# Optimization experiments

Hardware: AMD Instinct MI355X
Metric: run time of the kernel (lower is better)

The kernel has to match this reference:

```python
import jax, jax.numpy as jnp
import numpy as np

N, DIM = 32768, 2048
SPARSITY = 0.05
K = max(1, int(N * SPARSITY))  # 1638


def setup_inputs() -> dict:
    key = jax.random.key(0)
    ks = jax.random.split(key, 6)
    s = 1.0 / np.sqrt(DIM)
    return {
        "x": jax.random.normal(ks[0], (N, DIM), dtype=jnp.float32),
        "W1": jax.random.uniform(ks[1], (DIM, DIM), jnp.float32, -s, s),
        "b1": jax.random.uniform(ks[2], (DIM,), jnp.float32, -s, s),
        "W2": jax.random.uniform(ks[3], (DIM, DIM), jnp.float32, -s, s),
        "b2": jax.random.uniform(ks[4], (DIM,), jnp.float32, -s, s),
        "Wg": jax.random.uniform(ks[5], (DIM,), jnp.float32, -s, s),
        "bg": jnp.zeros((), jnp.float32),
    }


def reference(x, W1, b1, W2, b2, Wg, bg):
    # gate scores per row: [N]
    gate_scores = x @ Wg + bg
    # select top-k rows (k is static)
    _, top_idx = jax.lax.top_k(gate_scores, K)
    # gather active rows and run the 2-layer MLP only on them
    active_x = x[top_idx]                                   # [K, DIM]
    h = jax.nn.relu(active_x @ W1 + b1)
    active_out = h @ W2 + b2                                # [K, DIM]
    # scatter results back into a zero output; row order is irrelevant
    output = jnp.zeros_like(x).at[top_idx].set(active_out)
    mask = jnp.zeros((x.shape[0],), x.dtype).at[top_idx].set(1.0)
    return output, mask
```

## Files before the change

### kernel.cpp

```cpp
#include <hip/hip_runtime.h>

#define N_ROWS 32768
#define DIM    2048
#define KSEL   1638
#define MPAD   1664
#define GTILE  416

typedef __attribute__((ext_vector_type(4))) float          f32x4;
typedef __attribute__((ext_vector_type(4))) unsigned short us4;
typedef __attribute__((ext_vector_type(8))) unsigned short us8;
typedef __bf16 bf16x8 __attribute__((ext_vector_type(8)));

__device__ __forceinline__ unsigned short f2bf(float f) {
    unsigned u = __float_as_uint(f);
    u += 0x7FFFu + ((u >> 16) & 1u);
    return (unsigned short)(u >> 16);
}

__device__ __forceinline__ void gload_lds16(const void* g, void* l) {
    __builtin_amdgcn_global_load_lds(
        (const __attribute__((address_space(1))) unsigned int*)(uintptr_t)g,
        (__attribute__((address_space(3))) unsigned int*)(uintptr_t)l, 16, 0, 0);
}


__global__ __launch_bounds__(256) void prep_k(const float* __restrict__ x,
                                              const float* __restrict__ Wg,
                                              const float* __restrict__ bg,
                                              float* __restrict__ scores,
                                              const float* __restrict__ W1,
                                              const float* __restrict__ W2,
                                              unsigned short* __restrict__ W1t,
                                              unsigned short* __restrict__ W2t) {
    __shared__ unsigned short tile[64][72];
    const int b = blockIdx.x;
    const int t = threadIdx.x;
    if (b < 8192) {
        const int lane = t & 63, wid = t >> 6;
        const int row = b * 4 + wid;
        const float* xr = x + (size_t)row * DIM;
        float acc = 0.f;
#pragma unroll
        for (int i = 0; i < 8; ++i) {
            const int c = i * 256 + lane * 4;
            f32x4 a = __builtin_nontemporal_load((const f32x4*)&xr[c]);
            f32x4 w = *(const f32x4*)&Wg[c];
#pragma unroll
            for (int j = 0; j < 4; ++j) acc = fmaf(a[j], w[j], acc);
        }
#pragma unroll
        for (int off = 32; off >= 1; off >>= 1) acc += __shfl_down(acc, off);
        if (lane == 0) scores[row] = acc + bg[0];
    } else {
        const int cb = b - 8192;
        const int z = cb >> 10;
        const int rem = cb & 1023;
        const int k0 = (rem & 31) * 64;
        const int n0 = (rem >> 5) * 64;
        const float* W = z ? W2 : W1;
        unsigned short* Wt = z ? W2t : W1t;
        {
            const int r = t >> 4, c = (t & 15) * 4;
#pragma unroll
            for (int p = 0; p < 4; ++p) {
                const int rr = p * 16 + r;
                f32x4 v = *(const f32x4*)&W[(size_t)(k0 + rr) * DIM + n0 + c];
#pragma unroll
                for (int j = 0; j < 4; ++j) tile[rr][c + j] = f2bf(v[j]);
            }
        }
        __syncthreads();
        {
            const int n = t >> 4, kk = (t & 15) * 4;
#pragma unroll
            for (int p = 0; p < 4; ++p) {
                const int nn = p * 16 + n;
                us4 o;
#pragma unroll
                for (int j = 0; j < 4; ++j) o[j] = tile[kk + j][nn];
                *(us4*)&Wt[(size_t)(n0 + nn) * DIM + k0 + kk] = o;
            }
        }
    }
}

__global__ __launch_bounds__(1024) void select_k(const float* __restrict__ scores,
                                                 int* __restrict__ sel) {
    const int t = threadIdx.x;
    const int lane = t & 63, wid = t >> 6;
    unsigned key[32];
    unsigned kmin = 0xFFFFFFFFu, kmax = 0u;
#pragma unroll
    for (int i = 0; i < 8; ++i) {
        f32x4 v = *(const f32x4*)&scores[t * 32 + i * 4];
#pragma unroll
        for (int j = 0; j < 4; ++j) {
            unsigned u = __float_as_uint(v[j]);
            u = (u & 0x80000000u) ? ~u : (u | 0x80000000u);
            key[i * 4 + j] = u;
            kmin = min(kmin, u);
            kmax = max(kmax, u);
        }
    }
#pragma unroll
    for (int off = 32; off >= 1; off >>= 1) {
        kmin = min(kmin, (unsigned)__shfl_down((int)kmin, off));
        kmax = max(kmax, (unsigned)__shfl_down((int)kmax, off));
    }
    __shared__ unsigned wmin[16], wmax[16];
    __shared__ unsigned cnt[40];
    __shared__ unsigned gmin, gmax;
    if (t < 40) cnt[t] = 0u;
    if (lane == 0) { wmin[wid] = kmin; wmax[wid] = kmax; }
    __syncthreads();
    if (t == 0) {
        unsigned mn = wmin[0], mx = wmax[0];
        for (int w = 1; w < 16; ++w) { mn = min(mn, wmin[w]); mx = max(mx, wmax[w]); }
        gmin = mn; gmax = mx;
    }
    __syncthreads();
    unsigned lo = gmin, hi = gmax;
    int it = 0;
    while (lo < hi) {
        const unsigned mid = (unsigned)(((unsigned long long)lo + hi + 1ull) >> 1);
        int c = 0;
#pragma unroll
        for (int i = 0; i < 32; ++i) c += (key[i] >= mid) ? 1 : 0;
#pragma unroll
        for (int off = 32; off >= 1; off >>= 1) c += __shfl_down(c, off);
        if (lane == 0) atomicAdd(&cnt[it], (unsigned)c);
        __syncthreads();
        const unsigned total = cnt[it];
        if (total >= (unsigned)KSEL) lo = mid; else hi = mid - 1;
        ++it;
    }
    const unsigned kv = lo;
    __shared__ unsigned ctr, ectr;
    __shared__ int eq[256];
    if (t == 0) { ctr = 0; ectr = 0; }
    __syncthreads();
#pragma unroll
    for (int i = 0; i < 32; ++i) {
        const unsigned k = key[i];
        if (k > kv) {
            unsigned p = atomicAdd(&ctr, 1u);
            sel[p] = t * 32 + i;
        } else if (k == kv) {
            unsigned p = atomicAdd(&ectr, 1u);
            if (p < 256u) eq[p] = t * 32 + i;
        }
    }
    __syncthreads();
    if (t == 0) {
        const int C = (int)ctr;
        const int R = KSEL - C;
        const int E = (int)(ectr < 256u ? ectr : 256u);
        for (int r = 0; r < R; ++r) {
            int mi = r;
            for (int j = r + 1; j < E; ++j)
                if (eq[j] < eq[mi]) mi = j;
            int tmp = eq[r]; eq[r] = eq[mi]; eq[mi] = tmp;
            sel[C + r] = eq[r];
        }
    }
}

__global__ __launch_bounds__(256) void gather_k(const float* __restrict__ x,
                                                const int* __restrict__ sel,
                                                unsigned short* __restrict__ Abf,
                                                float* __restrict__ mask) {
    const int b = blockIdx.x, t = threadIdx.x;
    unsigned short* dst = Abf + (size_t)b * DIM + t * 8;
    if (b < KSEL) {
        const int src = sel[b];
        if (t == 0) mask[src] = 1.0f;
        const float* xr = x + (size_t)src * DIM + t * 8;
        f32x4 v0 = *(const f32x4*)xr;
        f32x4 v1 = *(const f32x4*)(xr + 4);
        us8 o;
#pragma unroll
        for (int j = 0; j < 4; ++j) { o[j] = f2bf(v0[j]); o[j + 4] = f2bf(v1[j]); }
        *(us8*)dst = o;
    } else {
        us8 z = {};
        *(us8*)dst = z;
    }
}

template <int EPI>
__global__ __launch_bounds__(256, 2) void gemm_k(const unsigned short* __restrict__ A,
                                                 const unsigned short* __restrict__ Bt,
                                                 const float* __restrict__ bias,
                                                 unsigned short* __restrict__ Hout,
                                                 float* __restrict__ Cout,
                                                 const int* __restrict__ sel) {
    __shared__ unsigned short lA[2][128 * 64];
    __shared__ unsigned short lB[2][64 * 64];
    const int t = threadIdx.x;
    const int lane = t & 63;
    const int wid = t >> 6;
    const int swz = (blockIdx.x & 7) * 52 + (blockIdx.x >> 3);
    const int m0 = (swz % 13) * 128;
    const int n0 = (swz / 13) * 64;
    const int wm = (wid >> 1) * 64;
    const int wn = (wid & 1) * 32;

    f32x4 acc[4][2] = {};

    const unsigned short *gA[4], *gB[2];
    int la[4], lb[2];
#pragma unroll
    for (int i = 0; i < 4; ++i) {
        const int e = t + i * 256, r = e >> 3;
        gA[i] = A + (size_t)(m0 + r) * DIM + ((e & 7) ^ (r & 7)) * 8;
        la[i] = e * 8;
    }
#pragma unroll
    for (int i = 0; i < 2; ++i) {
        const int e = t + i * 256, r = e >> 3;
        gB[i] = Bt + (size_t)(n0 + r) * DIM + ((e & 7) ^ (r & 7)) * 8;
        lb[i] = e * 8;
    }

    const int pc0 = (((lane >> 4) + 0) ^ (lane & 7)) * 8;
    const int pc1 = (((lane >> 4) + 4) ^ (lane & 7)) * 8;
    const int aob = (wm + (lane & 15)) * 64;
    const int bob = (wn + (lane & 15)) * 64;

#pragma unroll
    for (int i = 0; i < 4; ++i) gload_lds16(gA[i], &lA[0][la[i]]);
#pragma unroll
    for (int i = 0; i < 2; ++i) gload_lds16(gB[i], &lB[0][lb[i]]);
    __syncthreads();

    int cur = 0;
    for (int k0 = 0; k0 < DIM; k0 += 64) {
        if (k0 + 64 < DIM) {
            const int nxt = cur ^ 1, kn = k0 + 64;
#pragma unroll
            for (int i = 0; i < 4; ++i) gload_lds16(gA[i] + kn, &lA[nxt][la[i]]);
#pragma unroll
            for (int i = 0; i < 2; ++i) gload_lds16(gB[i] + kn, &lB[nxt][lb[i]]);
        }
        bf16x8 af0[4], af1[4], bf0[2], bf1[2];
#pragma unroll
        for (int mf = 0; mf < 4; ++mf) {
            af0[mf] = *(const bf16x8*)&lA[cur][aob + mf * 1024 + pc0];
            af1[mf] = *(const bf16x8*)&lA[cur][aob + mf * 1024 + pc1];
        }
#pragma unroll
        for (int nf = 0; nf < 2; ++nf) {
            bf0[nf] = *(const bf16x8*)&lB[cur][bob + nf * 1024 + pc0];
            bf1[nf] = *(const bf16x8*)&lB[cur][bob + nf * 1024 + pc1];
        }
#pragma unroll
        for (int mf = 0; mf < 4; ++mf)
#pragma unroll
            for (int nf = 0; nf < 2; ++nf)
                acc[mf][nf] = __builtin_amdgcn_mfma_f32_16x16x32_bf16(
                    af0[mf], bf0[nf], acc[mf][nf], 0, 0, 0);
#pragma unroll
        for (int mf = 0; mf < 4; ++mf)
#pragma unroll
            for (int nf = 0; nf < 2; ++nf)
                acc[mf][nf] = __builtin_amdgcn_mfma_f32_16x16x32_bf16(
                    af1[mf], bf1[nf], acc[mf][nf], 0, 0, 0);
        __syncthreads();
        cur ^= 1;
    }

#pragma unroll
    for (int mf = 0; mf < 4; ++mf) {
        const int rbase = m0 + wm + mf * 16 + (lane >> 4) * 4;
#pragma unroll
        for (int nf = 0; nf < 2; ++nf) {
            const int col = n0 + wn + nf * 16 + (lane & 15);
            const float bv = bias[col];
            if (EPI == 0) {
#pragma unroll
                for (int j = 0; j < 4; ++j) {
                    float v = acc[mf][nf][j] + bv;
                    v = fmaxf(v, 0.f);
                    Hout[(size_t)(rbase + j) * DIM + col] = f2bf(v);
                }
            } else {
#pragma unroll
                for (int j = 0; j < 4; ++j) {
                    const int r = rbase + j;
                    if (r < KSEL) {
                        __builtin_nontemporal_store(
                            acc[mf][nf][j] + bv,
                            &Cout[(size_t)sel[r] * DIM + col]);
                    }
                }
            }
        }
    }
}

extern "C" void kernel_launch(void* const* d_in, const int* in_sizes, int n_in,
                              void* d_out, int out_size, void* d_ws, size_t ws_size,
                              hipStream_t stream) {
    const float* x  = (const float*)d_in[0];
    const float* W1 = (const float*)d_in[1];
    const float* b1 = (const float*)d_in[2];
    const float* W2 = (const float*)d_in[3];
    const float* b2 = (const float*)d_in[4];
    const float* Wg = (const float*)d_in[5];
    const float* bg = (const float*)d_in[6];
    float* out  = (float*)d_out;
    float* mask = out + (size_t)N_ROWS * DIM;

    char* w = (char*)d_ws;
    float* scores = (float*)w;           w += (size_t)N_ROWS * 4;
    int* sel = (int*)w;                  w += 2048 * 4;
    unsigned short* Abf = (unsigned short*)w;  w += (size_t)MPAD * DIM * 2;
    unsigned short* Hbf = (unsigned short*)w;  w += (size_t)MPAD * DIM * 2;
    unsigned short* W1t = (unsigned short*)w;  w += (size_t)DIM * DIM * 2;
    unsigned short* W2t = (unsigned short*)w;  w += (size_t)DIM * DIM * 2;

    hipLaunchKernelGGL(prep_k, dim3(8192 + 2048), dim3(256), 0, stream,
                       x, Wg, bg, scores, W1, W2, W1t, W2t);
    hipLaunchKernelGGL(select_k, dim3(1), dim3(1024), 0, stream, scores, sel);
    hipLaunchKernelGGL(gather_k, dim3(MPAD), dim3(256), 0, stream, x, sel, Abf, mask);
    hipLaunchKernelGGL((gemm_k<0>), dim3(GTILE), dim3(256), 0, stream,
                       Abf, W1t, b1, Hbf, (float*)nullptr, (const int*)nullptr);
    hipLaunchKernelGGL((gemm_k<1>), dim3(GTILE), dim3(256), 0, stream,
                       Hbf, W2t, b2, (unsigned short*)nullptr, out, sel);
}
```

Measured before the change: 140.3 us.

## Radix-select top-k threshold and overlap it with weight transpose conversion

Replaces the binary-search threshold search, about 32 rounds of count plus barrier, with a three-pass radix histogram select (11/11/10 bits) that uses wave-level prefix scans. The gate-score computation is split into its own kernel. The weight bf16 transpose blocks move into the same launch as the single-block selection, so selection runs alongside the conversion instead of waiting behind it. The cost is LDS atomic contention on the histograms and a larger 1024-thread block for the transpose work.

```diff
diff --git a/kernel.cpp b/kernel.cpp
--- a/kernel.cpp
+++ b/kernel.cpp
@@ -24,35 +24,71 @@
 }
 
 
-__global__ __launch_bounds__(256) void prep_k(const float* __restrict__ x,
+__global__ __launch_bounds__(256) void gate_k(const float* __restrict__ x,
                                               const float* __restrict__ Wg,
                                               const float* __restrict__ bg,
-                                              float* __restrict__ scores,
-                                              const float* __restrict__ W1,
-                                              const float* __restrict__ W2,
-                                              unsigned short* __restrict__ W1t,
-                                              unsigned short* __restrict__ W2t) {
-    __shared__ unsigned short tile[64][72];
-    const int b = blockIdx.x;
+                                              float* __restrict__ scores) {
     const int t = threadIdx.x;
-    if (b < 8192) {
-        const int lane = t & 63, wid = t >> 6;
-        const int row = b * 4 + wid;
-        const float* xr = x + (size_t)row * DIM;
-        float acc = 0.f;
-#pragma unroll
-        for (int i = 0; i < 8; ++i) {
-            const int c = i * 256 + lane * 4;
-            f32x4 a = __builtin_nontemporal_load((const f32x4*)&xr[c]);
-            f32x4 w = *(const f32x4*)&Wg[c];
-#pragma unroll
-            for (int j = 0; j < 4; ++j) acc = fmaf(a[j], w[j], acc);
-        }
-#pragma unroll
-        for (int off = 32; off >= 1; off >>= 1) acc += __shfl_down(acc, off);
-        if (lane == 0) scores[row] = acc + bg[0];
-    } else {
-        const int cb = b - 8192;
+    const int lane = t & 63, wid = t >> 6;
+    const int row = blockIdx.x * 4 + wid;
+    const float* xr = x + (size_t)row * DIM;
+    float acc = 0.f;
+#pragma unroll
+    for (int i = 0; i < 8; ++i) {
+        const int c = i * 256 + lane * 4;
+        f32x4 a = __builtin_nontemporal_load((const f32x4*)&xr[c]);
+        f32x4 w = *(const f32x4*)&Wg[c];
+#pragma unroll
+        for (int j = 0; j < 4; ++j) acc = fmaf(a[j], w[j], acc);
+    }
+#pragma unroll
+    for (int off = 32; off >= 1; off >>= 1) acc += __shfl_down(acc, off);
+    if (lane == 0) scores[row] = acc + bg[0];
+}
+
+__device__ __forceinline__ void wave_find(const unsigned* hist, int per,
+                                          unsigned need, int lane,
+                                          int* ob, unsigned* oabove) {
+    unsigned g = 0;
+    for (int i = 0; i < per; ++i) g += hist[lane * per + i];
+    unsigned s = g;
+#pragma unroll
+    for (int d = 1; d < 64; d <<= 1) {
+        unsigned v = (unsigned)__shfl_down((int)s, d);
+        if (lane + d < 64) s += v;
+    }
+    const unsigned long long m = __ballot(s >= need);
+    const int gb = 63 - __builtin_clzll(m);
+    const unsigned above_g = (unsigned)__shfl((int)(s - g), gb);
+    const unsigned need2 = need - above_g;
+    unsigned h = (lane < per) ? hist[gb * per + lane] : 0u;
+    unsigned s2 = h;
+#pragma unroll
+    for (int d = 1; d < 64; d <<= 1) {
+        unsigned v = (unsigned)__shfl_down((int)s2, d);
+        if (lane + d < 64) s2 += v;
+    }
+    const unsigned long long m2 = __ballot(s2 >= need2);
+    const int bb = 63 - __builtin_clzll(m2);
+    const unsigned above_b = (unsigned)__shfl((int)(s2 - h), bb);
+    *ob = gb * per + bb;
+    *oabove = above_g + above_b;
+}
+
+__global__ __launch_bounds__(1024) void selconvt_k(const float* __restrict__ scores,
+                                                   int* __restrict__ sel,
+                                                   const float* __restrict__ W1,
+                                                   const float* __restrict__ W2,
+                                                   unsigned short* __restrict__ W1t,
+                                                   unsigned short* __restrict__ W2t) {
+    __shared__ unsigned short tile[4][64][72];
+    __shared__ unsigned hist[2048];
+    __shared__ unsigned bcb, bcn;
+    const int t = threadIdx.x;
+
+    if (blockIdx.x > 0) {
+        const int sb = t >> 8, t8 = t & 255;
+        const int cb = (blockIdx.x - 1) * 4 + sb;
         const int z = cb >> 10;
         const int rem = cb & 1023;
         const int k0 = (rem & 31) * 64;
@@ -60,36 +96,32 @@
         const float* W = z ? W2 : W1;
         unsigned short* Wt = z ? W2t : W1t;
         {
-            const int r = t >> 4, c = (t & 15) * 4;
+            const int r = t8 >> 4, c = (t8 & 15) * 4;
 #pragma unroll
             for (int p = 0; p < 4; ++p) {
                 const int rr = p * 16 + r;
                 f32x4 v = *(const f32x4*)&W[(size_t)(k0 + rr) * DIM + n0 + c];
 #pragma unroll
-                for (int j = 0; j < 4; ++j) tile[rr][c + j] = f2bf(v[j]);
+                for (int j = 0; j < 4; ++j) tile[sb][rr][c + j] = f2bf(v[j]);
             }
         }
         __syncthreads();
         {
-            const int n = t >> 4, kk = (t & 15) * 4;
+            const int n = t8 >> 4, kk = (t8 & 15) * 4;
 #pragma unroll
             for (int p = 0; p < 4; ++p) {
                 const int nn = p * 16 + n;
                 us4 o;
 #pragma unroll
-                for (int j = 0; j < 4; ++j) o[j] = tile[kk + j][nn];
+                for (int j = 0; j < 4; ++j) o[j] = tile[sb][kk + j][nn];
                 *(us4*)&Wt[(size_t)(n0 + nn) * DIM + k0 + kk] = o;
             }
         }
-    }
-}
-
-__global__ __launch_bounds__(1024) void select_k(const float* __restrict__ scores,
-                                                 int* __restrict__ sel) {
-    const int t = threadIdx.x;
-    const int lane = t & 63, wid = t >> 6;
+        return;
+    }
+
+    const int lane = t & 63;
     unsigned key[32];
-    unsigned kmin = 0xFFFFFFFFu, kmax = 0u;
 #pragma unroll
     for (int i = 0; i < 8; ++i) {
         f32x4 v = *(const f32x4*)&scores[t * 32 + i * 4];
@@ -98,43 +130,47 @@
             unsigned u = __float_as_uint(v[j]);
             u = (u & 0x80000000u) ? ~u : (u | 0x80000000u);
             key[i * 4 + j] = u;
-            kmin = min(kmin, u);
-            kmax = max(kmax, u);
-        }
-    }
-#pragma unroll
-    for (int off = 32; off >= 1; off >>= 1) {
-        kmin = min(kmin, (unsigned)__shfl_down((int)kmin, off));
-        kmax = max(kmax, (unsigned)__shfl_down((int)kmax, off));
-    }
-    __shared__ unsigned wmin[16], wmax[16];
-    __shared__ unsigned cnt[40];
-    __shared__ unsigned gmin, gmax;
-    if (t < 40) cnt[t] = 0u;
-    if (lane == 0) { wmin[wid] = kmin; wmax[wid] = kmax; }
-    __syncthreads();
-    if (t == 0) {
-        unsigned mn = wmin[0], mx = wmax[0];
-        for (int w = 1; w < 16; ++w) { mn = min(mn, wmin[w]); mx = max(mx, wmax[w]); }
-        gmin = mn; gmax = mx;
-    }
-    __syncthreads();
-    unsigned lo = gmin, hi = gmax;
-    int it = 0;
-    while (lo < hi) {
-        const unsigned mid = (unsigned)(((unsigned long long)lo + hi + 1ull) >> 1);
-        int c = 0;
-#pragma unroll
-        for (int i = 0; i < 32; ++i) c += (key[i] >= mid) ? 1 : 0;
-#pragma unroll
-        for (int off = 32; off >= 1; off >>= 1) c += __shfl_down(c, off);
-        if (lane == 0) atomicAdd(&cnt[it], (unsigned)c);
-        __syncthreads();
-        const unsigned total = cnt[it];
-        if (total >= (unsigned)KSEL) lo = mid; else hi = mid - 1;
-        ++it;
-    }
-    const unsigned kv = lo;
+        }
+    }
+    hist[t] = 0u; hist[t + 1024] = 0u;
+    __syncthreads();
+#pragma unroll
+    for (int i = 0; i < 32; ++i) atomicAdd(&hist[key[i] >> 21], 1u);
+    __syncthreads();
+    if (t < 64) {
+        int b; unsigned ab;
+        wave_find(hist, 32, KSEL, lane, &b, &ab);
+        if (t == 0) { bcb = (unsigned)b; bcn = KSEL - ab; }
+    }
+    __syncthreads();
+    const unsigned p1 = bcb; const unsigned need2 = bcn;
+    hist[t] = 0u; hist[t + 1024] = 0u;
+    __syncthreads();
+#pragma unroll
+    for (int i = 0; i < 32; ++i)
+        if ((key[i] >> 21) == p1) atomicAdd(&hist[(key[i] >> 10) & 0x7FFu], 1u);
+    __syncthreads();
+    if (t < 64) {
+        int b; unsigned ab;
+        wave_find(hist, 32, need2, lane, &b, &ab);
+        if (t == 0) { bcb = (unsigned)b; bcn = need2 - ab; }
+    }
+    __syncthreads();
+    const unsigned p2 = (p1 << 11) | bcb; const unsigned need3 = bcn;
+    hist[t] = 0u; hist[t + 1024] = 0u;
+    __syncthreads();
+#pragma unroll
+    for (int i = 0; i < 32; ++i)
+        if ((key[i] >> 10) == p2) atomicAdd(&hist[key[i] & 0x3FFu], 1u);
+    __syncthreads();
+    if (t < 64) {
+        int b; unsigned ab;
+        wave_find(hist, 16, need3, lane, &b, &ab);
+        if (t == 0) bcb = (unsigned)b;
+    }
+    __syncthreads();
+    const unsigned kv = (p2 << 10) | bcb;
+
     __shared__ unsigned ctr, ectr;
     __shared__ int eq[256];
     if (t == 0) { ctr = 0; ectr = 0; }
@@ -319,9 +355,10 @@
     unsigned short* W1t = (unsigned short*)w;  w += (size_t)DIM * DIM * 2;
     unsigned short* W2t = (unsigned short*)w;  w += (size_t)DIM * DIM * 2;
 
-    hipLaunchKernelGGL(prep_k, dim3(8192 + 2048), dim3(256), 0, stream,
-                       x, Wg, bg, scores, W1, W2, W1t, W2t);
-    hipLaunchKernelGGL(select_k, dim3(1), dim3(1024), 0, stream, scores, sel);
+    hipLaunchKernelGGL(gate_k, dim3(N_ROWS / 4), dim3(256), 0, stream,
+                       x, Wg, bg, scores);
+    hipLaunchKernelGGL(selconvt_k, dim3(513), dim3(1024), 0, stream,
+                       scores, sel, W1, W2, W1t, W2t);
     hipLaunchKernelGGL(gather_k, dim3(MPAD), dim3(256), 0, stream, x, sel, Abf, mask);
     hipLaunchKernelGGL((gemm_k<0>), dim3(GTILE), dim3(256), 0, stream,
                        Abf, W1t, b1, Hbf, (float*)nullptr, (const int*)nullptr);
```

New measurement: 114.9 us (median of 2 runs). 1.22x faster.
